# Kernel optimization log

Measured on AMD Instinct MI355X. Metric: run time of the kernel, lower is better.

The kernel has to match this reference:

```python
import jax, jax.numpy as jnp
import numpy as np

NMS_PRE, NMS_POST, NMS_THRESH = 1024, 512, 0.7
B, A, FEAT = 4, 70400, 27648
BN_EPS = 1e-5


def _bev_iou(boxes):
    # boxes: [K, 7] (x, y, z, dx, dy, dz, ry); axis-aligned BEV IoU
    x, y, dx, dy = boxes[:, 0], boxes[:, 1], boxes[:, 3], boxes[:, 4]
    x1, x2 = x - 0.5 * dx, x + 0.5 * dx
    y1, y2 = y - 0.5 * dy, y + 0.5 * dy
    iw = jnp.clip(jnp.minimum(x2[:, None], x2[None, :]) - jnp.maximum(x1[:, None], x1[None, :]), 0.0)
    ih = jnp.clip(jnp.minimum(y2[:, None], y2[None, :]) - jnp.maximum(y1[:, None], y1[None, :]), 0.0)
    inter = iw * ih
    area = dx * dy
    return inter / jnp.clip(area[:, None] + area[None, :] - inter, 1e-6)


def _greedy_nms(boxes, thresh):
    # boxes sorted by score desc; returns keep mask [K]
    K = boxes.shape[0]
    iou = _bev_iou(boxes)
    idx = jnp.arange(K)

    def step(keep, i):
        sup = (iou[i] > thresh) & (idx > i) & keep[i]
        return keep & ~sup, None

    keep, _ = jax.lax.scan(step, jnp.ones(K, dtype=bool), jnp.arange(K))
    return keep


def _proposal_one(box, cls):
    # box: [A, 7], cls: [A, n_cls]  ->  padded rois [NPOST,7], scores [NPOST], labels [NPOST]
    score = jnp.max(cls, axis=-1)
    label = jnp.argmax(cls, axis=-1)
    top_score, top_idx = jax.lax.top_k(score, NMS_PRE)
    top_box = box[top_idx]
    keep = _greedy_nms(top_box, NMS_THRESH)
    # stable: kept entries first, preserving score order
    order = jnp.argsort(jnp.where(keep, jnp.arange(NMS_PRE), NMS_PRE + jnp.arange(NMS_PRE)))
    sel = order[:NMS_POST]
    valid = jnp.arange(NMS_POST) < jnp.minimum(jnp.sum(keep), NMS_POST)
    rois = jnp.where(valid[:, None], top_box[sel], 0.0)
    roi_score = jnp.where(valid, top_score[sel], 0.0)
    roi_label = jnp.where(valid, label[top_idx][sel], 0) + 1  # +1 as in module
    return rois, roi_score, roi_label


def _bn_relu(h, g, b):
    # eval-mode BN with running_mean=0, running_var=1
    return jax.nn.relu(h * (g / jnp.sqrt(1.0 + BN_EPS)) + b)


def _decode(reg, anchors):
    # ResidualCoder_v1.decode_torch
    xa, ya, za = anchors[..., 0], anchors[..., 1], anchors[..., 2]
    dxa, dya, dza, ra = anchors[..., 3], anchors[..., 4], anchors[..., 5], anchors[..., 6]
    xt, yt, zt = reg[..., 0], reg[..., 1], reg[..., 2]
    dxt, dyt, dzt, rt = reg[..., 3], reg[..., 4], reg[..., 5], reg[..., 6]
    diag = jnp.sqrt(dxa * dxa + dya * dya)
    return jnp.stack([
        xt * diag + xa, yt * diag + ya, zt * dza + za,
        jnp.exp(dxt) * dxa, jnp.exp(dyt) * dya, jnp.exp(dzt) * dza,
        rt + ra], axis=-1)


def _rotate_z(box, ang):
    # rotate x,y of box [..., 7] by ang [...]
    c, s = jnp.cos(ang), jnp.sin(ang)
    x = box[..., 0] * c - box[..., 1] * s
    y = box[..., 0] * s + box[..., 1] * c
    return jnp.concatenate([x[..., None], y[..., None], box[..., 2:]], axis=-1)


def reference(rpn_box_preds, rpn_cls_preds, pooled_features,
              Ws1, g1, b1, Ws2, g2, b2,
              Wc1, gc1, bc1, Wc2, gc2, bc2, Wc3, bc3,
              Wr1, gr1, br1, Wr2, gr2, br2, Wr3, br3):
    # proposal_layer: per-batch topk + NMS + padded scatter (vmapped)
    rois, roi_scores, roi_labels = jax.vmap(_proposal_one)(rpn_box_preds, rpn_cls_preds)

    # shared / cls / reg heads (1x1 Conv1d == per-roi MLP), dropout off (eval)
    x = _bn_relu(pooled_features @ Ws1.T, g1, b1)
    x = _bn_relu(x @ Ws2.T, g2, b2)
    c = _bn_relu(x @ Wc1.T, gc1, bc1)
    c = _bn_relu(c @ Wc2.T, gc2, bc2)
    cls_preds = c @ Wc3.T + bc3          # [B*NPOST, 1]
    r = _bn_relu(x @ Wr1.T, gr1, br1)
    r = _bn_relu(r @ Wr2.T, gr2, br2)
    reg_preds = r @ Wr3.T + br3          # [B*NPOST, 7]

    bsz = rois.shape[0]
    cls_preds = cls_preds.reshape(bsz, -1, cls_preds.shape[-1])
    reg_preds = reg_preds.reshape(bsz, -1, 7)

    # generate_predict_box: decode against detached rois with xyz zeroed
    anchors = jax.lax.stop_gradient(rois)
    anchors = anchors.at[..., 0:3].set(0.0)
    box_ct = _decode(reg_preds, anchors)
    box_preds = _rotate_z(box_ct, rois[..., 6])
    box_preds = jnp.concatenate([box_preds[..., 0:3] + rois[..., 0:3], box_preds[..., 3:]], axis=-1)

    return jnp.concatenate([cls_preds, box_preds, roi_scores[..., None]], axis=-1)  # [B, NPOST, 9]


def setup_inputs():
    key = jax.random.key(0)
    ks = jax.random.split(key, 32)
    u = jax.random.uniform(ks[0], (B, A, 7), dtype=jnp.float32)
    lo = jnp.array([0.0, -40.0, -2.0, 1.5, 1.4, 1.0, -3.14159], jnp.float32)
    hi = jnp.array([70.0, 40.0, 0.0, 4.5, 2.0, 2.0, 3.14159], jnp.float32)
    rpn_box_preds = lo + u * (hi - lo)
    rpn_cls_preds = jax.random.normal(ks[1], (B, A, 3), dtype=jnp.float32)
    pooled_features = jax.random.normal(ks[2], (B * NMS_POST, FEAT), dtype=jnp.float32) * 0.1

    def w(k, o, i, std=None):
        s = (1.0 / np.sqrt(i)) if std is None else std
        return jax.random.normal(k, (o, i), dtype=jnp.float32) * s

    d = dict(
        rpn_box_preds=rpn_box_preds, rpn_cls_preds=rpn_cls_preds, pooled_features=pooled_features,
        Ws1=w(ks[3], 256, FEAT), g1=jnp.ones(256), b1=jnp.zeros(256),
        Ws2=w(ks[4], 256, 256), g2=jnp.ones(256), b2=jnp.zeros(256),
        Wc1=w(ks[5], 256, 256), gc1=jnp.ones(256), bc1=jnp.zeros(256),
        Wc2=w(ks[6], 256, 256), gc2=jnp.ones(256), bc2=jnp.zeros(256),
        Wc3=w(ks[7], 1, 256), bc3=jnp.zeros(1),
        Wr1=w(ks[8], 256, 256), gr1=jnp.ones(256), br1=jnp.zeros(256),
        Wr2=w(ks[9], 256, 256), gr2=jnp.ones(256), br2=jnp.zeros(256),
        Wr3=w(ks[10], 7, 256, std=0.001), br3=jnp.zeros(7),
    )
    return d
```

## Files before the change

kernel.cpp:

```cpp
#include <hip/hip_runtime.h>
#include <cstdint>

typedef unsigned int u32;
typedef unsigned long long u64;
typedef unsigned short u16;

#define BATCH 4
#define A_CNT 70400
#define FEAT 27648
#define KSPLIT 16
#define KCHUNK 1728
#define NTILE_IT 27

typedef __attribute__((ext_vector_type(8))) short bf16x8;
typedef __attribute__((ext_vector_type(4))) float f32x4;
typedef __attribute__((ext_vector_type(4))) u32 u32x4;

constexpr size_t OF_KEYS = 0;
constexpr size_t OF_TBOX = OF_KEYS + 1126400;
constexpr size_t OF_TSC  = OF_TBOX + 114688;
constexpr size_t OF_BX1  = OF_TSC + 16384;
constexpr size_t OF_BX2  = OF_BX1 + 16384;
constexpr size_t OF_BY1  = OF_BX2 + 16384;
constexpr size_t OF_BY2  = OF_BY1 + 16384;
constexpr size_t OF_BAR  = OF_BY2 + 16384;
constexpr size_t OF_MASK = OF_BAR + 16384;
constexpr size_t OF_ROIS = OF_MASK + 524288;
constexpr size_t OF_RSC  = OF_ROIS + 57344;
constexpr size_t OF_BSW  = OF_RSC + 8192;
constexpr size_t OF_PART = OF_BSW + 14155776;
constexpr size_t WS_NEED = OF_PART + 33554432;

__device__ __forceinline__ u32 keyOf(float f) {
  u32 u = __float_as_uint(f);
  return (u & 0x80000000u) ? ~u : (u | 0x80000000u);
}
__device__ __forceinline__ float keyToF(u32 k) {
  u32 u = (k & 0x80000000u) ? (k ^ 0x80000000u) : ~k;
  return __uint_as_float(u);
}
__device__ __forceinline__ u16 f2bf(float f) {
  u32 u = __float_as_uint(f);
  u32 r = 0x7FFFu + ((u >> 16) & 1u);
  return (u16)((u + r) >> 16);
}
__device__ __forceinline__ void gload_lds16(const void* g, void* l) {
  auto gp = reinterpret_cast<const __attribute__((address_space(1))) unsigned int*>(
      reinterpret_cast<uintptr_t>(g));
  auto lp = reinterpret_cast<__attribute__((address_space(3))) unsigned int*>(
      reinterpret_cast<uintptr_t>(l));
  __builtin_amdgcn_global_load_lds(gp, lp, 16, 0, 0);
}
__device__ __forceinline__ u64 shflx64(u64 v, int m) {
  u32 lo = (u32)v, hi = (u32)(v >> 32);
  lo = __shfl_xor(lo, m, 64);
  hi = __shfl_xor(hi, m, 64);
  return ((u64)hi << 32) | lo;
}
__device__ __forceinline__ u32x4 pack8(float4 a, float4 b) {
  u32x4 o;
  o.x = (u32)f2bf(a.x) | ((u32)f2bf(a.y) << 16);
  o.y = (u32)f2bf(a.z) | ((u32)f2bf(a.w) << 16);
  o.z = (u32)f2bf(b.x) | ((u32)f2bf(b.y) << 16);
  o.w = (u32)f2bf(b.z) | ((u32)f2bf(b.w) << 16);
  return o;
}
__device__ __forceinline__ bf16x8 cvt8(float4 a, float4 b) {
  u32x4 p = pack8(a, b);
  return *(bf16x8*)&p;
}

__global__ __launch_bounds__(1024) void k_fatA(const float* __restrict__ cls,
    const float* __restrict__ Ws1, u32* __restrict__ keys, u32* __restrict__ Bsw)
{
  int bid = blockIdx.x;
  int t = threadIdx.x;
  if (bid < 864) {
    u32 w = (u32)bid * 1024u + t;
    u32 tile = w >> 11;
    u32 rem = w & 2047u;
    u32 n = rem >> 3;
    u32 pq = (rem & 7u) << 4;
    u32 q0 = pq ^ ((n & 7u) << 4);
    u32 col0 = tile * 64u + (q0 >> 1);
    const float* src = Ws1 + (size_t)n * FEAT + col0;
    float4 f0 = *(const float4*)src;
    float4 f1 = *(const float4*)(src + 4);
    ((u32x4*)Bsw)[w] = pack8(f0, f1);
    return;
  }
  u32 g = (u32)(bid - 864) * 1024u + t;
  float s0 = cls[(size_t)g * 3 + 0];
  float s1 = cls[(size_t)g * 3 + 1];
  float s2 = cls[(size_t)g * 3 + 2];
  keys[g] = keyOf(fmaxf(s0, fmaxf(s1, s2)));
}

__global__ __launch_bounds__(1024) void k_prop(const u32* __restrict__ keys,
    const float* __restrict__ boxes, float* __restrict__ tbox, float* __restrict__ tsc,
    float* __restrict__ bx1, float* __restrict__ bx2, float* __restrict__ by1,
    float* __restrict__ by2, float* __restrict__ bar)
{
  int b = blockIdx.x, t = threadIdx.x;
  int lane = t & 63, wv = t >> 6;
  const u32* kb = keys + (size_t)b * A_CNT;
  __shared__ u64 s[2048];
  __shared__ u32 partials[16];
  __shared__ u32 cc;
  u32 h[35];
#pragma unroll
  for (int j = 0; j < 35; ++j) {
    int g0 = t + ((2 * j) << 10);
    int g1 = t + ((2 * j + 1) << 10);
    u32 a = (g0 < A_CNT) ? (kb[g0] >> 16) : 0u;
    u32 c2 = (g1 < A_CNT) ? (kb[g1] >> 16) : 0u;
    h[j] = a | (c2 << 16);
  }
  if (t == 0) cc = 0u;
  u32 lo = 0, hi = 65536;
  while (hi - lo > 1) {
    u32 mid = (lo + hi) >> 1;
    u32 c = 0;
#pragma unroll
    for (int j = 0; j < 35; ++j) {
      c += ((h[j] & 0xFFFFu) >= mid) ? 1u : 0u;
      c += ((h[j] >> 16) >= mid) ? 1u : 0u;
    }
#pragma unroll
    for (int o = 32; o > 0; o >>= 1) c += __shfl_xor(c, o, 64);
    __syncthreads();
    if (lane == 0) partials[wv] = c;
    __syncthreads();
    u32 tot = 0;
#pragma unroll
    for (int w2 = 0; w2 < 16; ++w2) tot += partials[w2];
    if (tot >= 1024u) lo = mid; else hi = mid;
  }
  u32 kth = lo;
  __syncthreads();
  u32 kc = kb[t];
#pragma unroll 1
  for (int i = 0; i < 69; ++i) {
    int g = t + (i << 10);
    u32 k = kc;
    if (i < 68) {
      int gn = t + ((i + 1) << 10);
      kc = (gn < A_CNT) ? kb[gn] : 0u;
    }
    bool pass = (g < A_CNT) && ((k >> 16) >= kth);
    u64 mm = __ballot(pass);
    if (mm) {
      int leader = __ffsll((unsigned long long)mm) - 1;
      u32 base = 0;
      if (lane == leader) base = atomicAdd(&cc, (u32)__popcll(mm));
      base = __shfl(base, leader, 64);
      if (pass) {
        u32 pos = base + (u32)__popcll(mm & ((1ull << lane) - 1ull));
        if (pos < 2048u) s[pos] = ((u64)k << 32) | (u32)(~(u32)g);
      }
    }
  }
  __syncthreads();
  u32 m = cc; if (m > 2048u) m = 2048u;
  for (int e = t; e < 2048; e += 1024) if (e >= (int)m) s[e] = 0ull;
  __syncthreads();
  {
    u64 v0 = s[2 * t], v1 = s[2 * t + 1];
#pragma unroll
    for (u32 k = 2; k <= 128; k <<= 1) {
      bool desc = ((t & (k >> 1)) == 0);
#pragma unroll
      for (u32 j = (k >> 1); j >= 2; j >>= 1) {
        u32 mmk = j >> 1;
        u64 p0 = shflx64(v0, mmk);
        u64 p1 = shflx64(v1, mmk);
        bool up = ((t & mmk) == 0);
        bool mx = (desc == up);
        v0 = mx ? (v0 > p0 ? v0 : p0) : (v0 < p0 ? v0 : p0);
        v1 = mx ? (v1 > p1 ? v1 : p1) : (v1 < p1 ? v1 : p1);
      }
      if (desc ? (v0 < v1) : (v0 > v1)) { u64 tmp = v0; v0 = v1; v1 = tmp; }
    }
    s[2 * t] = v0; s[2 * t + 1] = v1;
    __syncthreads();
    for (u32 k = 256; k <= 2048; k <<= 1) {
      for (u32 j = k >> 1; j >= 128; j >>= 1) {
        for (int e = t; e < 2048; e += 1024) {
          u32 p = (u32)e ^ j;
          if (p > (u32)e) {
            bool d2 = ((e & k) == 0);
            u64 x = s[e], y = s[p];
            if (d2 ? (x < y) : (x > y)) { s[e] = y; s[p] = x; }
          }
        }
        __syncthreads();
      }
      u64 v0 = s[2 * t], v1 = s[2 * t + 1];
      bool desc = ((t & (k >> 1)) == 0);
#pragma unroll
      for (u32 j = 64; j >= 2; j >>= 1) {
        u32 mmk = j >> 1;
        u64 p0 = shflx64(v0, mmk);
        u64 p1 = shflx64(v1, mmk);
        bool up = ((t & mmk) == 0);
        bool mx = (desc == up);
        v0 = mx ? (v0 > p0 ? v0 : p0) : (v0 < p0 ? v0 : p0);
        v1 = mx ? (v1 > p1 ? v1 : p1) : (v1 < p1 ? v1 : p1);
      }
      if (desc ? (v0 < v1) : (v0 > v1)) { u64 tmp = v0; v0 = v1; v1 = tmp; }
      s[2 * t] = v0; s[2 * t + 1] = v1;
      __syncthreads();
    }
  }
  u64 comp = s[t];
  u32 kk = (u32)(comp >> 32);
  u32 a = ~(u32)(comp & 0xFFFFFFFFull);
  int o = b * 1024 + t;
  tsc[o] = keyToF(kk);
  const float* bp = boxes + ((size_t)b * A_CNT + a) * 7;
  float x = bp[0], y = bp[1], z = bp[2], dx = bp[3], dy = bp[4], dz = bp[5], rr = bp[6];
  float* tb = tbox + (size_t)o * 7;
  tb[0] = x; tb[1] = y; tb[2] = z; tb[3] = dx; tb[4] = dy; tb[5] = dz; tb[6] = rr;
  {
#pragma clang fp contract(off)
    bx1[o] = x - 0.5f * dx; bx2[o] = x + 0.5f * dx;
    by1[o] = y - 0.5f * dy; by2[o] = y + 0.5f * dy;
    bar[o] = dx * dy;
  }
}

__global__ __launch_bounds__(256) void k_fatB(const float* __restrict__ A,
    const u32* __restrict__ Bsw, float* __restrict__ part,
    const float* __restrict__ bx1, const float* __restrict__ bx2,
    const float* __restrict__ by1, const float* __restrict__ by2,
    const float* __restrict__ bar, u32* __restrict__ mask)
{
  __shared__ __align__(16) char smem[65536];
  int bid = blockIdx.x;
  if (bid >= 512) {
    int mi = bid - 512;
    int b = mi >> 6;
    int cbk = (mi >> 2) & 15;
    int rb0 = (mi & 3) * 4;
    int tt = threadIdx.x;
    int rbi = tt >> 6, ln = tt & 63;
    int r = (rb0 + rbi) * 64 + ln;
    int o = b * 1024, jc0 = cbk * 64;
    float* cx1 = (float*)(smem);
    float* cx2 = (float*)(smem + 256);
    float* cy1 = (float*)(smem + 512);
    float* cy2 = (float*)(smem + 768);
    float* car = (float*)(smem + 1024);
    if (tt < 64) {
      cx1[tt] = bx1[o + jc0 + tt]; cx2[tt] = bx2[o + jc0 + tt];
      cy1[tt] = by1[o + jc0 + tt]; cy2[tt] = by2[o + jc0 + tt];
      car[tt] = bar[o + jc0 + tt];
    }
    __syncthreads();
    float rx1 = bx1[o + r], rx2 = bx2[o + r], ry1 = by1[o + r], ry2 = by2[o + r], rar = bar[o + r];
    u32 w0 = 0, w1 = 0;
    {
#pragma clang fp contract(off)
      for (int c = 0; c < 64; ++c) {
        int jc = jc0 + c;
        float iw = fminf(rx2, cx2[c]) - fmaxf(rx1, cx1[c]); iw = fmaxf(iw, 0.0f);
        float ih = fminf(ry2, cy2[c]) - fmaxf(ry1, cy1[c]); ih = fmaxf(ih, 0.0f);
        float inter = iw * ih;
        float den = fmaxf(rar + car[c] - inter, 1e-6f);
        float iou = inter / den;
        if ((iou > 0.7f) && (jc > r)) {
          if (c < 32) w0 |= 1u << c; else w1 |= 1u << (c - 32);
        }
      }
    }
    mask[((size_t)(o + r)) * 32 + cbk * 2 + 0] = w0;
    mask[((size_t)(o + r)) * 32 + cbk * 2 + 1] = w1;
    return;
  }
  int q = bid >> 3;
  int ks = (bid & 7) * 2 + (q >> 5);
  int mt = q & 31;
  int tid = threadIdx.x, lane = tid & 63, wv = tid >> 6;
  int row16 = lane & 15, kgrp = lane >> 4;

  f32x4 acc[16];
#pragma unroll
  for (int i = 0; i < 16; ++i) acc[i] = (f32x4){0.f, 0.f, 0.f, 0.f};

  const float* aptr = A + ((size_t)(mt * 64 + wv * 16 + row16)) * FEAT
                        + (size_t)ks * KCHUNK + kgrp * 8;
  const char* bsrc_base = (const char*)Bsw + ((size_t)(ks * NTILE_IT)) * 32768 + (wv * 8) * 1024 + lane * 16;
  int bdoff = (wv * 8) * 1024;

  int boff[16][2];
#pragma unroll
  for (int ksub = 0; ksub < 2; ++ksub) {
    int qq = ksub * 64 + kgrp * 16;
#pragma unroll
    for (int nf = 0; nf < 16; ++nf) {
      int n = nf * 16 + row16;
      boff[nf][ksub] = n * 128 + (qq ^ ((n & 7) << 4));
    }
  }

  bf16x8 a0, a1;
  {
    const float4* ap = (const float4*)aptr;
    float4 g0 = ap[0], g1 = ap[1];
    const float4* ap2 = (const float4*)(aptr + 32);
    float4 g2 = ap2[0], g3 = ap2[1];
    a0 = cvt8(g0, g1);
    a1 = cvt8(g2, g3);
#pragma unroll
    for (int i = 0; i < 8; ++i)
      gload_lds16(bsrc_base + i * 1024, smem + bdoff + i * 1024);
  }
  __syncthreads();

  for (int it = 0; it < NTILE_IT; ++it) {
    char* Bcur = smem + ((it & 1) ? 32768 : 0);
    char* Bnxt = smem + ((it & 1) ? 0 : 32768);
    bool has = (it + 1 < NTILE_IT);
    float4 g0, g1, g2, g3;
    if (has) {
      const float* an = aptr + (it + 1) * 64;
      const float4* ap = (const float4*)an;
      g0 = ap[0]; g1 = ap[1];
      const float4* ap2 = (const float4*)(an + 32);
      g2 = ap2[0]; g3 = ap2[1];
      const char* bs = bsrc_base + (size_t)(it + 1) * 32768;
#pragma unroll
      for (int i = 0; i < 8; ++i)
        gload_lds16(bs + i * 1024, Bnxt + bdoff + i * 1024);
    }
#pragma unroll
    for (int nf = 0; nf < 16; ++nf) {
      bf16x8 b0 = *(const bf16x8*)(Bcur + boff[nf][0]);
      acc[nf] = __builtin_amdgcn_mfma_f32_16x16x32_bf16(a0, b0, acc[nf], 0, 0, 0);
      bf16x8 b1 = *(const bf16x8*)(Bcur + boff[nf][1]);
      acc[nf] = __builtin_amdgcn_mfma_f32_16x16x32_bf16(a1, b1, acc[nf], 0, 0, 0);
    }
    if (has) {
      a0 = cvt8(g0, g1);
      a1 = cvt8(g2, g3);
    }
    __syncthreads();
  }
  float* pb = part + (size_t)ks * 524288;
  int orow = mt * 64 + wv * 16 + kgrp * 4;
#pragma unroll
  for (int nf = 0; nf < 16; ++nf) {
    int col = nf * 16 + row16;
#pragma unroll
    for (int rr = 0; rr < 4; ++rr)
      pb[(size_t)(orow + rr) * 256 + col] = acc[nf][rr];
  }
}

__global__ __launch_bounds__(64) void k_nms(const u32* __restrict__ mask,
    const float* __restrict__ tbox, const float* __restrict__ tsc,
    float* __restrict__ rois, float* __restrict__ rsc)
{
  int b = blockIdx.x;
  int lane = threadIdx.x;
  int el = lane & 31;
  const u32* M = mask + (size_t)b * 1024 * 32;
  u32 R = 0;
  u32 cur[32], nxt[32];
#pragma unroll
  for (int i = 0; i < 32; ++i) cur[i] = M[(size_t)(i * 32 + el)];
#pragma unroll 1
  for (int c = 0; c < 32; ++c) {
    if (c < 31) {
      int nb = (c + 1) * 1024 + el;
#pragma unroll
      for (int i = 0; i < 32; ++i) nxt[i] = M[(size_t)(nb + i * 32)];
    }
    u32 w = R;
#pragma unroll
    for (int i = 0; i < 32; ++i) w |= ((w >> i) & 1u) ? 0u : cur[i];
    u32 wfin = __shfl(w, c, 64);
#pragma unroll
    for (int i = 0; i < 32; ++i) R |= ((wfin >> i) & 1u) ? 0u : cur[i];
#pragma unroll
    for (int i = 0; i < 32; ++i) cur[i] = nxt[i];
  }
  u32 keepw = (lane < 32) ? ~R : 0u;
  int c = __popc(keepw);
  int pre = c;
  for (int d = 1; d < 64; d <<= 1) {
    int v = __shfl_up(pre, d, 64);
    if (lane >= d) pre += v;
  }
  int total = __shfl(pre, 31, 64);
  int base = pre - c;
  if (lane < 32) {
    u32 w = keepw;
    int rank = base;
    while (w) {
      int bit = __ffs(w) - 1;
      w &= w - 1;
      if (rank < 512) {
        int r = lane * 32 + bit;
        const float* tb = tbox + ((size_t)b * 1024 + r) * 7;
        float* rp = rois + ((size_t)b * 512 + rank) * 7;
        rp[0] = tb[0]; rp[1] = tb[1]; rp[2] = tb[2]; rp[3] = tb[3];
        rp[4] = tb[4]; rp[5] = tb[5]; rp[6] = tb[6];
        rsc[b * 512 + rank] = tsc[b * 1024 + r];
      }
      rank++;
    }
  }
  for (int z = total + lane; z < 512; z += 64) {
    float* rp = rois + ((size_t)b * 512 + z) * 7;
    rp[0] = rp[1] = rp[2] = rp[3] = rp[4] = rp[5] = rp[6] = 0.0f;
    rsc[b * 512 + z] = 0.0f;
  }
}

__device__ __forceinline__ void layer4(const float (*IN)[256], const float* __restrict__ W,
    const float* __restrict__ g, const float* __restrict__ bb, float (*OUT)[256], int t, int h)
{
  float acc[4] = {0, 0, 0, 0};
  const float* Wrow = W + (size_t)t * 256;
  for (int k = 0; k < 256; k += 4) {
    float4 w4 = *(const float4*)&Wrow[k];
#pragma unroll
    for (int r = 0; r < 4; ++r) {
      float4 xv = *(const float4*)&IN[h * 4 + r][k];
      acc[r] = fmaf(xv.x, w4.x, acc[r]);
      acc[r] = fmaf(xv.y, w4.y, acc[r]);
      acc[r] = fmaf(xv.z, w4.z, acc[r]);
      acc[r] = fmaf(xv.w, w4.w, acc[r]);
    }
  }
  float sc = g[t] / sqrtf(1.0f + 1e-5f);
  float bv = bb[t];
#pragma unroll
  for (int r = 0; r < 4; ++r)
    OUT[h * 4 + r][t] = fmaxf(fmaf(acc[r], sc, bv), 0.0f);
}

__global__ __launch_bounds__(512) void k_chain(const float* __restrict__ part,
    const float* __restrict__ Ws2, const float* __restrict__ Wc1, const float* __restrict__ Wc2,
    const float* __restrict__ Wr1, const float* __restrict__ Wr2,
    const float* __restrict__ g1, const float* __restrict__ b1,
    const float* __restrict__ g2, const float* __restrict__ b2,
    const float* __restrict__ gc1, const float* __restrict__ bc1,
    const float* __restrict__ gc2, const float* __restrict__ bc2,
    const float* __restrict__ gr1, const float* __restrict__ br1,
    const float* __restrict__ gr2, const float* __restrict__ br2,
    const float* __restrict__ Wc3, const float* __restrict__ bc3,
    const float* __restrict__ Wr3, const float* __restrict__ br3,
    const float* __restrict__ rois, const float* __restrict__ rsc,
    float* __restrict__ out)
{
  int bid = blockIdx.x, tid = threadIdx.x;
  int t = tid & 255, h = tid >> 8;
  __shared__ __align__(16) float bufX[8][256];
  __shared__ __align__(16) float bufY[8][256];
  __shared__ __align__(16) float bufC[8][256];
  __shared__ __align__(16) float bufR[8][256];
  __shared__ float hd[64];
  {
    float sc = g1[t] / sqrtf(1.0f + 1e-5f);
    float bv = b1[t];
#pragma unroll
    for (int r = 0; r < 4; ++r) {
      int row = h * 4 + r;
      float s = 0.f;
#pragma unroll
      for (int ks = 0; ks < KSPLIT; ++ks)
        s += part[(size_t)ks * 524288 + (size_t)(bid * 8 + row) * 256 + t];
      bufX[row][t] = fmaxf(fmaf(s, sc, bv), 0.0f);
    }
  }
  __syncthreads();
  layer4(bufX, Ws2, g2, b2, bufY, t, h);
  __syncthreads();
  layer4(bufY, Wc1, gc1, bc1, bufC, t, h);
  layer4(bufY, Wr1, gr1, br1, bufR, t, h);
  __syncthreads();
  layer4(bufC, Wc2, gc2, bc2, bufX, t, h);
  layer4(bufR, Wr2, gr2, br2, bufY, t, h);
  __syncthreads();
  int wv = tid >> 6, ln = tid & 63;
  for (int task = wv; task < 64; task += 8) {
    float p;
    if (task < 8) {
      float4 yv = *(const float4*)&bufX[task][ln * 4];
      float4 w4 = ((const float4*)Wc3)[ln];
      p = yv.x * w4.x + yv.y * w4.y + yv.z * w4.z + yv.w * w4.w;
    } else {
      int i = task - 8, row = i / 7, j = i % 7;
      float4 yv = *(const float4*)&bufY[row][ln * 4];
      float4 w4 = ((const float4*)(Wr3 + j * 256))[ln];
      p = yv.x * w4.x + yv.y * w4.y + yv.z * w4.z + yv.w * w4.w;
    }
#pragma unroll
    for (int off = 32; off > 0; off >>= 1) p += __shfl_xor(p, off, 64);
    if (ln == 0) hd[task] = p;
  }
  __syncthreads();
  if (tid < 8) {
    int m = bid * 8 + tid;
    float clsv = hd[tid] + bc3[0];
    float rg[7];
#pragma unroll
    for (int j = 0; j < 7; ++j) rg[j] = hd[8 + tid * 7 + j] + br3[j];
    const float* R = rois + (size_t)m * 7;
    float rx = R[0], ry = R[1], rz = R[2], dxa = R[3], dya = R[4], dza = R[5], ra = R[6];
    float diag = sqrtf(dxa * dxa + dya * dya);
    float x = rg[0] * diag, y = rg[1] * diag, z = rg[2] * dza;
    float ex = expf(rg[3]) * dxa, ey = expf(rg[4]) * dya, ez = expf(rg[5]) * dza;
    float hr = rg[6] + ra;
    float cc = cosf(ra), sn = sinf(ra);
    float xr = x * cc - y * sn, yr = x * sn + y * cc;
    float* O = out + (size_t)m * 9;
    O[0] = clsv; O[1] = xr + rx; O[2] = yr + ry; O[3] = z + rz;
    O[4] = ex; O[5] = ey; O[6] = ez; O[7] = hr; O[8] = rsc[m];
  }
}

extern "C" void kernel_launch(void* const* d_in, const int* in_sizes, int n_in,
                              void* d_out, int out_size, void* d_ws, size_t ws_size,
                              hipStream_t stream)
{
  const float* rpn_box = (const float*)d_in[0];
  const float* rpn_cls = (const float*)d_in[1];
  const float* pooled  = (const float*)d_in[2];
  const float* Ws1 = (const float*)d_in[3];
  const float* g1  = (const float*)d_in[4];
  const float* b1  = (const float*)d_in[5];
  const float* Ws2 = (const float*)d_in[6];
  const float* g2  = (const float*)d_in[7];
  const float* b2  = (const float*)d_in[8];
  const float* Wc1 = (const float*)d_in[9];
  const float* gc1 = (const float*)d_in[10];
  const float* bc1 = (const float*)d_in[11];
  const float* Wc2 = (const float*)d_in[12];
  const float* gc2 = (const float*)d_in[13];
  const float* bc2 = (const float*)d_in[14];
  const float* Wc3 = (const float*)d_in[15];
  const float* bc3 = (const float*)d_in[16];
  const float* Wr1 = (const float*)d_in[17];
  const float* gr1 = (const float*)d_in[18];
  const float* br1 = (const float*)d_in[19];
  const float* Wr2 = (const float*)d_in[20];
  const float* gr2 = (const float*)d_in[21];
  const float* br2 = (const float*)d_in[22];
  const float* Wr3 = (const float*)d_in[23];
  const float* br3 = (const float*)d_in[24];

  if (ws_size < WS_NEED) return;

  char* ws = (char*)d_ws;
  u32* keys = (u32*)(ws + OF_KEYS);
  float* tbox = (float*)(ws + OF_TBOX);
  float* tsc  = (float*)(ws + OF_TSC);
  float* bx1 = (float*)(ws + OF_BX1);
  float* bx2 = (float*)(ws + OF_BX2);
  float* by1 = (float*)(ws + OF_BY1);
  float* by2 = (float*)(ws + OF_BY2);
  float* bar = (float*)(ws + OF_BAR);
  u32* mask = (u32*)(ws + OF_MASK);
  float* roisb = (float*)(ws + OF_ROIS);
  float* rscb  = (float*)(ws + OF_RSC);
  u32* Bsw = (u32*)(ws + OF_BSW);
  float* part = (float*)(ws + OF_PART);

  k_fatA<<<1139, 1024, 0, stream>>>(rpn_cls, Ws1, keys, Bsw);
  k_prop<<<4, 1024, 0, stream>>>(keys, rpn_box, tbox, tsc, bx1, bx2, by1, by2, bar);
  k_fatB<<<768, 256, 0, stream>>>(pooled, Bsw, part, bx1, bx2, by1, by2, bar, mask);
  k_nms<<<4, 64, 0, stream>>>(mask, tbox, tsc, roisb, rscb);
  k_chain<<<256, 512, 0, stream>>>(part, Ws2, Wc1, Wc2, Wr1, Wr2,
                                   g1, b1, g2, b2, gc1, bc1, gc2, bc2,
                                   gr1, br1, gr2, br2, Wc3, bc3, Wr3, br3,
                                   roisb, rscb, (float*)d_out);
}
```

Baseline: 266.1 us.

## Fuse top-k proposal selection with the big GEMM and split IoU mask kernel

The 4-block proposal/top-k kernel is merged into the large split-K GEMM launch, so the serial sort runs alongside GEMM blocks instead of in its own near-empty launch. The GEMM tile is restructured into 1024-thread blocks: 16 waves each own a 16-column slice, and the A tile is staged in LDS as bf16 while B is double-buffered in LDS. The IoU mask computation moves out of the GEMM kernel into its own 1024-thread kernel that runs after proposal selection. The restructured GEMM adds extra barriers per iteration and uses 72KB of LDS per block, which may lower occupancy, and the mask work now costs an additional launch.

```diff
diff --git a/kernel.cpp b/kernel.cpp
--- a/kernel.cpp
+++ b/kernel.cpp
@@ -14,6 +14,7 @@
 
 typedef __attribute__((ext_vector_type(8))) short bf16x8;
 typedef __attribute__((ext_vector_type(4))) float f32x4;
+typedef __attribute__((ext_vector_type(2))) u32 u32x2;
 typedef __attribute__((ext_vector_type(4))) u32 u32x4;
 
 constexpr size_t OF_KEYS = 0;
@@ -64,10 +65,6 @@
   o.z = (u32)f2bf(b.x) | ((u32)f2bf(b.y) << 16);
   o.w = (u32)f2bf(b.z) | ((u32)f2bf(b.w) << 16);
   return o;
-}
-__device__ __forceinline__ bf16x8 cvt8(float4 a, float4 b) {
-  u32x4 p = pack8(a, b);
-  return *(bf16x8*)&p;
 }
 
 __global__ __launch_bounds__(1024) void k_fatA(const float* __restrict__ cls,
@@ -96,265 +93,267 @@
   keys[g] = keyOf(fmaxf(s0, fmaxf(s1, s2)));
 }
 
-__global__ __launch_bounds__(1024) void k_prop(const u32* __restrict__ keys,
-    const float* __restrict__ boxes, float* __restrict__ tbox, float* __restrict__ tsc,
+__global__ __launch_bounds__(1024) void k_big(const u32* __restrict__ keys,
+    const float* __restrict__ boxes, const float* __restrict__ A,
+    const u32* __restrict__ Bsw, float* __restrict__ part,
+    float* __restrict__ tbox, float* __restrict__ tsc,
     float* __restrict__ bx1, float* __restrict__ bx2, float* __restrict__ by1,
     float* __restrict__ by2, float* __restrict__ bar)
 {
-  int b = blockIdx.x, t = threadIdx.x;
-  int lane = t & 63, wv = t >> 6;
-  const u32* kb = keys + (size_t)b * A_CNT;
-  __shared__ u64 s[2048];
-  __shared__ u32 partials[16];
-  __shared__ u32 cc;
-  u32 h[35];
-#pragma unroll
-  for (int j = 0; j < 35; ++j) {
-    int g0 = t + ((2 * j) << 10);
-    int g1 = t + ((2 * j + 1) << 10);
-    u32 a = (g0 < A_CNT) ? (kb[g0] >> 16) : 0u;
-    u32 c2 = (g1 < A_CNT) ? (kb[g1] >> 16) : 0u;
-    h[j] = a | (c2 << 16);
-  }
-  if (t == 0) cc = 0u;
-  u32 lo = 0, hi = 65536;
-  while (hi - lo > 1) {
-    u32 mid = (lo + hi) >> 1;
-    u32 c = 0;
+  __shared__ __align__(16) char smem[73728];
+  int bid = blockIdx.x;
+  int t = threadIdx.x;
+  if (bid < 4) {
+    int b = bid;
+    int lane = t & 63, wv = t >> 6;
+    const u32* kb = keys + (size_t)b * A_CNT;
+    u64* s = (u64*)smem;
+    u32* partials = (u32*)(smem + 16384);
+    u32* ccp = (u32*)(smem + 16448);
+    u32 h[35];
 #pragma unroll
     for (int j = 0; j < 35; ++j) {
-      c += ((h[j] & 0xFFFFu) >= mid) ? 1u : 0u;
-      c += ((h[j] >> 16) >= mid) ? 1u : 0u;
-    }
-#pragma unroll
-    for (int o = 32; o > 0; o >>= 1) c += __shfl_xor(c, o, 64);
+      int g0 = t + ((2 * j) << 10);
+      int g1 = t + ((2 * j + 1) << 10);
+      u32 a = (g0 < A_CNT) ? (kb[g0] >> 16) : 0u;
+      u32 c2 = (g1 < A_CNT) ? (kb[g1] >> 16) : 0u;
+      h[j] = a | (c2 << 16);
+    }
+    if (t == 0) ccp[0] = 0u;
+    u32 lo = 0, hi = 65536;
+    while (hi - lo > 1) {
+      u32 mid = (lo + hi) >> 1;
+      u32 c = 0;
+#pragma unroll
+      for (int j = 0; j < 35; ++j) {
+        c += ((h[j] & 0xFFFFu) >= mid) ? 1u : 0u;
+        c += ((h[j] >> 16) >= mid) ? 1u : 0u;
+      }
+#pragma unroll
+      for (int o = 32; o > 0; o >>= 1) c += __shfl_xor(c, o, 64);
+      __syncthreads();
+      if (lane == 0) partials[wv] = c;
+      __syncthreads();
+      u32 tot = 0;
+#pragma unroll
+      for (int w2 = 0; w2 < 16; ++w2) tot += partials[w2];
+      if (tot >= 1024u) lo = mid; else hi = mid;
+    }
+    u32 kth = lo;
     __syncthreads();
-    if (lane == 0) partials[wv] = c;
+    u32 kc = kb[t];
+#pragma unroll 1
+    for (int i = 0; i < 69; ++i) {
+      int g = t + (i << 10);
+      u32 k = kc;
+      if (i < 68) {
+        int gn = t + ((i + 1) << 10);
+        kc = (gn < A_CNT) ? kb[gn] : 0u;
+      }
+      bool pass = (g < A_CNT) && ((k >> 16) >= kth);
+      u64 mm = __ballot(pass);
+      if (mm) {
+        int leader = __ffsll((unsigned long long)mm) - 1;
+        u32 base = 0;
+        if (lane == leader) base = atomicAdd(ccp, (u32)__popcll(mm));
+        base = __shfl(base, leader, 64);
+        if (pass) {
+          u32 pos = base + (u32)__popcll(mm & ((1ull << lane) - 1ull));
+          if (pos < 2048u) s[pos] = ((u64)k << 32) | (u32)(~(u32)g);
+        }
+      }
+    }
     __syncthreads();
-    u32 tot = 0;
-#pragma unroll
-    for (int w2 = 0; w2 < 16; ++w2) tot += partials[w2];
-    if (tot >= 1024u) lo = mid; else hi = mid;
-  }
-  u32 kth = lo;
-  __syncthreads();
-  u32 kc = kb[t];
-#pragma unroll 1
-  for (int i = 0; i < 69; ++i) {
-    int g = t + (i << 10);
-    u32 k = kc;
-    if (i < 68) {
-      int gn = t + ((i + 1) << 10);
-      kc = (gn < A_CNT) ? kb[gn] : 0u;
-    }
-    bool pass = (g < A_CNT) && ((k >> 16) >= kth);
-    u64 mm = __ballot(pass);
-    if (mm) {
-      int leader = __ffsll((unsigned long long)mm) - 1;
-      u32 base = 0;
-      if (lane == leader) base = atomicAdd(&cc, (u32)__popcll(mm));
-      base = __shfl(base, leader, 64);
-      if (pass) {
-        u32 pos = base + (u32)__popcll(mm & ((1ull << lane) - 1ull));
-        if (pos < 2048u) s[pos] = ((u64)k << 32) | (u32)(~(u32)g);
-      }
-    }
-  }
-  __syncthreads();
-  u32 m = cc; if (m > 2048u) m = 2048u;
-  for (int e = t; e < 2048; e += 1024) if (e >= (int)m) s[e] = 0ull;
-  __syncthreads();
-  {
-    u64 v0 = s[2 * t], v1 = s[2 * t + 1];
-#pragma unroll
-    for (u32 k = 2; k <= 128; k <<= 1) {
-      bool desc = ((t & (k >> 1)) == 0);
-#pragma unroll
-      for (u32 j = (k >> 1); j >= 2; j >>= 1) {
-        u32 mmk = j >> 1;
-        u64 p0 = shflx64(v0, mmk);
-        u64 p1 = shflx64(v1, mmk);
-        bool up = ((t & mmk) == 0);
-        bool mx = (desc == up);
-        v0 = mx ? (v0 > p0 ? v0 : p0) : (v0 < p0 ? v0 : p0);
-        v1 = mx ? (v1 > p1 ? v1 : p1) : (v1 < p1 ? v1 : p1);
-      }
-      if (desc ? (v0 < v1) : (v0 > v1)) { u64 tmp = v0; v0 = v1; v1 = tmp; }
-    }
-    s[2 * t] = v0; s[2 * t + 1] = v1;
+    u32 m = ccp[0]; if (m > 2048u) m = 2048u;
+    for (int e = t; e < 2048; e += 1024) if (e >= (int)m) s[e] = 0ull;
     __syncthreads();
-    for (u32 k = 256; k <= 2048; k <<= 1) {
-      for (u32 j = k >> 1; j >= 128; j >>= 1) {
-        for (int e = t; e < 2048; e += 1024) {
-          u32 p = (u32)e ^ j;
-          if (p > (u32)e) {
-            bool d2 = ((e & k) == 0);
-            u64 x = s[e], y = s[p];
-            if (d2 ? (x < y) : (x > y)) { s[e] = y; s[p] = x; }
-          }
+    {
+      u64 v0 = s[2 * t], v1 = s[2 * t + 1];
+#pragma unroll
+      for (u32 k = 2; k <= 128; k <<= 1) {
+        bool desc = ((t & (k >> 1)) == 0);
+#pragma unroll
+        for (u32 j = (k >> 1); j >= 2; j >>= 1) {
+          u32 mmk = j >> 1;
+          u64 p0 = shflx64(v0, mmk);
+          u64 p1 = shflx64(v1, mmk);
+          bool up = ((t & mmk) == 0);
+          bool mx = (desc == up);
+          v0 = mx ? (v0 > p0 ? v0 : p0) : (v0 < p0 ? v0 : p0);
+          v1 = mx ? (v1 > p1 ? v1 : p1) : (v1 < p1 ? v1 : p1);
         }
-        __syncthreads();
-      }
-      u64 v0 = s[2 * t], v1 = s[2 * t + 1];
-      bool desc = ((t & (k >> 1)) == 0);
-#pragma unroll
-      for (u32 j = 64; j >= 2; j >>= 1) {
-        u32 mmk = j >> 1;
-        u64 p0 = shflx64(v0, mmk);
-        u64 p1 = shflx64(v1, mmk);
-        bool up = ((t & mmk) == 0);
-        bool mx = (desc == up);
-        v0 = mx ? (v0 > p0 ? v0 : p0) : (v0 < p0 ? v0 : p0);
-        v1 = mx ? (v1 > p1 ? v1 : p1) : (v1 < p1 ? v1 : p1);
-      }
-      if (desc ? (v0 < v1) : (v0 > v1)) { u64 tmp = v0; v0 = v1; v1 = tmp; }
+        if (desc ? (v0 < v1) : (v0 > v1)) { u64 tmp = v0; v0 = v1; v1 = tmp; }
+      }
       s[2 * t] = v0; s[2 * t + 1] = v1;
       __syncthreads();
-    }
-  }
-  u64 comp = s[t];
-  u32 kk = (u32)(comp >> 32);
-  u32 a = ~(u32)(comp & 0xFFFFFFFFull);
-  int o = b * 1024 + t;
-  tsc[o] = keyToF(kk);
-  const float* bp = boxes + ((size_t)b * A_CNT + a) * 7;
-  float x = bp[0], y = bp[1], z = bp[2], dx = bp[3], dy = bp[4], dz = bp[5], rr = bp[6];
-  float* tb = tbox + (size_t)o * 7;
-  tb[0] = x; tb[1] = y; tb[2] = z; tb[3] = dx; tb[4] = dy; tb[5] = dz; tb[6] = rr;
+      for (u32 k = 256; k <= 2048; k <<= 1) {
+        for (u32 j = k >> 1; j >= 128; j >>= 1) {
+          for (int e = t; e < 2048; e += 1024) {
+            u32 p = (u32)e ^ j;
+            if (p > (u32)e) {
+              bool d2 = ((e & k) == 0);
+              u64 x = s[e], y = s[p];
+              if (d2 ? (x < y) : (x > y)) { s[e] = y; s[p] = x; }
+            }
+          }
+          __syncthreads();
+        }
+        u64 v0 = s[2 * t], v1 = s[2 * t + 1];
+        bool desc = ((t & (k >> 1)) == 0);
+#pragma unroll
+        for (u32 j = 64; j >= 2; j >>= 1) {
+          u32 mmk = j >> 1;
+          u64 p0 = shflx64(v0, mmk);
+          u64 p1 = shflx64(v1, mmk);
+          bool up = ((t & mmk) == 0);
+          bool mx = (desc == up);
+          v0 = mx ? (v0 > p0 ? v0 : p0) : (v0 < p0 ? v0 : p0);
+          v1 = mx ? (v1 > p1 ? v1 : p1) : (v1 < p1 ? v1 : p1);
+        }
+        if (desc ? (v0 < v1) : (v0 > v1)) { u64 tmp = v0; v0 = v1; v1 = tmp; }
+        s[2 * t] = v0; s[2 * t + 1] = v1;
+        __syncthreads();
+      }
+    }
+    u64 comp = s[t];
+    u32 kk = (u32)(comp >> 32);
+    u32 a = ~(u32)(comp & 0xFFFFFFFFull);
+    int o = b * 1024 + t;
+    tsc[o] = keyToF(kk);
+    const float* bp = boxes + ((size_t)b * A_CNT + a) * 7;
+    float x = bp[0], y = bp[1], z = bp[2], dx = bp[3], dy = bp[4], dz = bp[5], rr = bp[6];
+    float* tb = tbox + (size_t)o * 7;
+    tb[0] = x; tb[1] = y; tb[2] = z; tb[3] = dx; tb[4] = dy; tb[5] = dz; tb[6] = rr;
+    {
+#pragma clang fp contract(off)
+      bx1[o] = x - 0.5f * dx; bx2[o] = x + 0.5f * dx;
+      by1[o] = y - 0.5f * dy; by2[o] = y + 0.5f * dy;
+      bar[o] = dx * dy;
+    }
+    return;
+  }
+  int bid2 = bid - 4;
+  int q = bid2 >> 3;
+  int ks = (bid2 & 7) * 2 + (q >> 5);
+  int mt = q & 31;
+  int lane = t & 63, wvid = t >> 6;
+  int row16 = lane & 15, kgrp = lane >> 4;
+
+  f32x4 acc[4];
+#pragma unroll
+  for (int i = 0; i < 4; ++i) acc[i] = (f32x4){0.f, 0.f, 0.f, 0.f};
+
+  int arow = t >> 4;
+  int akb = (t & 15) * 4;
+  const float* ap_base = A + ((size_t)(mt * 64 + arow)) * FEAT + (size_t)ks * KCHUNK + akb;
+  int asw = (arow & 7) << 4;
+  int awoff = arow * 128 + (((t & 15) * 8) ^ asw);
+  const char* bsrc_base = (const char*)Bsw + ((size_t)(ks * NTILE_IT)) * 32768 + wvid * 2048 + lane * 16;
+  int bdoff = wvid * 2048 + lane * 16;
+  char* Albuf = smem;
+  char* Bbase = smem + 8192;
+
+  int aoff[4][2], boff[2];
+#pragma unroll
+  for (int ksub = 0; ksub < 2; ++ksub) {
+    int qq = ksub * 64 + kgrp * 16;
+#pragma unroll
+    for (int mf = 0; mf < 4; ++mf) {
+      int row = mf * 16 + row16;
+      aoff[mf][ksub] = row * 128 + (qq ^ ((row & 7) << 4));
+    }
+    int n = wvid * 16 + row16;
+    boff[ksub] = n * 128 + (qq ^ ((n & 7) << 4));
+  }
+
+  {
+    float4 ga = *(const float4*)ap_base;
+    u32x2 c;
+    c.x = (u32)f2bf(ga.x) | ((u32)f2bf(ga.y) << 16);
+    c.y = (u32)f2bf(ga.z) | ((u32)f2bf(ga.w) << 16);
+    *(u32x2*)(Albuf + awoff) = c;
+    gload_lds16(bsrc_base, Bbase + bdoff);
+    gload_lds16(bsrc_base + 1024, Bbase + bdoff + 1024);
+  }
+  __syncthreads();
+
+  for (int it = 0; it < NTILE_IT; ++it) {
+    char* Bcur = Bbase + ((it & 1) ? 32768 : 0);
+    char* Bnxt = Bbase + ((it & 1) ? 0 : 32768);
+    bool has = (it + 1 < NTILE_IT);
+    float4 ga;
+    if (has) ga = *(const float4*)(ap_base + (it + 1) * 64);
+    bf16x8 bf0 = *(const bf16x8*)(Bcur + boff[0]);
+    bf16x8 bf1 = *(const bf16x8*)(Bcur + boff[1]);
+    __syncthreads();
+    if (has) {
+      const char* bs = bsrc_base + (size_t)(it + 1) * 32768;
+      gload_lds16(bs, Bnxt + bdoff);
+      gload_lds16(bs + 1024, Bnxt + bdoff + 1024);
+    }
+#pragma unroll
+    for (int mf = 0; mf < 4; ++mf) {
+      bf16x8 a0 = *(const bf16x8*)(Albuf + aoff[mf][0]);
+      acc[mf] = __builtin_amdgcn_mfma_f32_16x16x32_bf16(a0, bf0, acc[mf], 0, 0, 0);
+      bf16x8 a1 = *(const bf16x8*)(Albuf + aoff[mf][1]);
+      acc[mf] = __builtin_amdgcn_mfma_f32_16x16x32_bf16(a1, bf1, acc[mf], 0, 0, 0);
+    }
+    __syncthreads();
+    if (has) {
+      u32x2 c;
+      c.x = (u32)f2bf(ga.x) | ((u32)f2bf(ga.y) << 16);
+      c.y = (u32)f2bf(ga.z) | ((u32)f2bf(ga.w) << 16);
+      *(u32x2*)(Albuf + awoff) = c;
+    }
+    __syncthreads();
+  }
+  float* pb = part + (size_t)ks * 524288;
+#pragma unroll
+  for (int mf = 0; mf < 4; ++mf) {
+    int orow = mt * 64 + mf * 16 + kgrp * 4;
+    int col = wvid * 16 + row16;
+#pragma unroll
+    for (int rr = 0; rr < 4; ++rr)
+      pb[(size_t)(orow + rr) * 256 + col] = acc[mf][rr];
+  }
+}
+
+__global__ __launch_bounds__(1024) void k_mask(const float* __restrict__ bx1,
+    const float* __restrict__ bx2, const float* __restrict__ by1,
+    const float* __restrict__ by2, const float* __restrict__ bar,
+    u32* __restrict__ mask)
+{
+  __shared__ float csm[16][5][64];
+  int tt = threadIdx.x;
+  int ug = tt >> 6, ln = tt & 63;
+  int unit = blockIdx.x * 16 + ug;
+  int b = unit >> 8, cbk = (unit >> 4) & 15, rb = unit & 15;
+  int o = b * 1024, jc0 = cbk * 64;
+  int r = rb * 64 + ln;
+  csm[ug][0][ln] = bx1[o + jc0 + ln];
+  csm[ug][1][ln] = bx2[o + jc0 + ln];
+  csm[ug][2][ln] = by1[o + jc0 + ln];
+  csm[ug][3][ln] = by2[o + jc0 + ln];
+  csm[ug][4][ln] = bar[o + jc0 + ln];
+  __syncthreads();
+  float rx1 = bx1[o + r], rx2 = bx2[o + r], ry1 = by1[o + r], ry2 = by2[o + r], rar = bar[o + r];
+  u32 w0 = 0, w1 = 0;
   {
 #pragma clang fp contract(off)
-    bx1[o] = x - 0.5f * dx; bx2[o] = x + 0.5f * dx;
-    by1[o] = y - 0.5f * dy; by2[o] = y + 0.5f * dy;
-    bar[o] = dx * dy;
-  }
-}
-
-__global__ __launch_bounds__(256) void k_fatB(const float* __restrict__ A,
-    const u32* __restrict__ Bsw, float* __restrict__ part,
-    const float* __restrict__ bx1, const float* __restrict__ bx2,
-    const float* __restrict__ by1, const float* __restrict__ by2,
-    const float* __restrict__ bar, u32* __restrict__ mask)
-{
-  __shared__ __align__(16) char smem[65536];
-  int bid = blockIdx.x;
-  if (bid >= 512) {
-    int mi = bid - 512;
-    int b = mi >> 6;
-    int cbk = (mi >> 2) & 15;
-    int rb0 = (mi & 3) * 4;
-    int tt = threadIdx.x;
-    int rbi = tt >> 6, ln = tt & 63;
-    int r = (rb0 + rbi) * 64 + ln;
-    int o = b * 1024, jc0 = cbk * 64;
-    float* cx1 = (float*)(smem);
-    float* cx2 = (float*)(smem + 256);
-    float* cy1 = (float*)(smem + 512);
-    float* cy2 = (float*)(smem + 768);
-    float* car = (float*)(smem + 1024);
-    if (tt < 64) {
-      cx1[tt] = bx1[o + jc0 + tt]; cx2[tt] = bx2[o + jc0 + tt];
-      cy1[tt] = by1[o + jc0 + tt]; cy2[tt] = by2[o + jc0 + tt];
-      car[tt] = bar[o + jc0 + tt];
-    }
-    __syncthreads();
-    float rx1 = bx1[o + r], rx2 = bx2[o + r], ry1 = by1[o + r], ry2 = by2[o + r], rar = bar[o + r];
-    u32 w0 = 0, w1 = 0;
-    {
-#pragma clang fp contract(off)
-      for (int c = 0; c < 64; ++c) {
-        int jc = jc0 + c;
-        float iw = fminf(rx2, cx2[c]) - fmaxf(rx1, cx1[c]); iw = fmaxf(iw, 0.0f);
-        float ih = fminf(ry2, cy2[c]) - fmaxf(ry1, cy1[c]); ih = fmaxf(ih, 0.0f);
-        float inter = iw * ih;
-        float den = fmaxf(rar + car[c] - inter, 1e-6f);
-        float iou = inter / den;
-        if ((iou > 0.7f) && (jc > r)) {
-          if (c < 32) w0 |= 1u << c; else w1 |= 1u << (c - 32);
-        }
-      }
-    }
-    mask[((size_t)(o + r)) * 32 + cbk * 2 + 0] = w0;
-    mask[((size_t)(o + r)) * 32 + cbk * 2 + 1] = w1;
-    return;
-  }
-  int q = bid >> 3;
-  int ks = (bid & 7) * 2 + (q >> 5);
-  int mt = q & 31;
-  int tid = threadIdx.x, lane = tid & 63, wv = tid >> 6;
-  int row16 = lane & 15, kgrp = lane >> 4;
-
-  f32x4 acc[16];
-#pragma unroll
-  for (int i = 0; i < 16; ++i) acc[i] = (f32x4){0.f, 0.f, 0.f, 0.f};
-
-  const float* aptr = A + ((size_t)(mt * 64 + wv * 16 + row16)) * FEAT
-                        + (size_t)ks * KCHUNK + kgrp * 8;
-  const char* bsrc_base = (const char*)Bsw + ((size_t)(ks * NTILE_IT)) * 32768 + (wv * 8) * 1024 + lane * 16;
-  int bdoff = (wv * 8) * 1024;
-
-  int boff[16][2];
-#pragma unroll
-  for (int ksub = 0; ksub < 2; ++ksub) {
-    int qq = ksub * 64 + kgrp * 16;
-#pragma unroll
-    for (int nf = 0; nf < 16; ++nf) {
-      int n = nf * 16 + row16;
-      boff[nf][ksub] = n * 128 + (qq ^ ((n & 7) << 4));
-    }
-  }
-
-  bf16x8 a0, a1;
-  {
-    const float4* ap = (const float4*)aptr;
-    float4 g0 = ap[0], g1 = ap[1];
-    const float4* ap2 = (const float4*)(aptr + 32);
-    float4 g2 = ap2[0], g3 = ap2[1];
-    a0 = cvt8(g0, g1);
-    a1 = cvt8(g2, g3);
-#pragma unroll
-    for (int i = 0; i < 8; ++i)
-      gload_lds16(bsrc_base + i * 1024, smem + bdoff + i * 1024);
-  }
-  __syncthreads();
-
-  for (int it = 0; it < NTILE_IT; ++it) {
-    char* Bcur = smem + ((it & 1) ? 32768 : 0);
-    char* Bnxt = smem + ((it & 1) ? 0 : 32768);
-    bool has = (it + 1 < NTILE_IT);
-    float4 g0, g1, g2, g3;
-    if (has) {
-      const float* an = aptr + (it + 1) * 64;
-      const float4* ap = (const float4*)an;
-      g0 = ap[0]; g1 = ap[1];
-      const float4* ap2 = (const float4*)(an + 32);
-      g2 = ap2[0]; g3 = ap2[1];
-      const char* bs = bsrc_base + (size_t)(it + 1) * 32768;
-#pragma unroll
-      for (int i = 0; i < 8; ++i)
-        gload_lds16(bs + i * 1024, Bnxt + bdoff + i * 1024);
-    }
-#pragma unroll
-    for (int nf = 0; nf < 16; ++nf) {
-      bf16x8 b0 = *(const bf16x8*)(Bcur + boff[nf][0]);
-      acc[nf] = __builtin_amdgcn_mfma_f32_16x16x32_bf16(a0, b0, acc[nf], 0, 0, 0);
-      bf16x8 b1 = *(const bf16x8*)(Bcur + boff[nf][1]);
-      acc[nf] = __builtin_amdgcn_mfma_f32_16x16x32_bf16(a1, b1, acc[nf], 0, 0, 0);
-    }
-    if (has) {
-      a0 = cvt8(g0, g1);
-      a1 = cvt8(g2, g3);
-    }
-    __syncthreads();
-  }
-  float* pb = part + (size_t)ks * 524288;
-  int orow = mt * 64 + wv * 16 + kgrp * 4;
-#pragma unroll
-  for (int nf = 0; nf < 16; ++nf) {
-    int col = nf * 16 + row16;
-#pragma unroll
-    for (int rr = 0; rr < 4; ++rr)
-      pb[(size_t)(orow + rr) * 256 + col] = acc[nf][rr];
-  }
+    for (int c = 0; c < 64; ++c) {
+      int jc = jc0 + c;
+      float iw = fminf(rx2, csm[ug][1][c]) - fmaxf(rx1, csm[ug][0][c]); iw = fmaxf(iw, 0.0f);
+      float ih = fminf(ry2, csm[ug][3][c]) - fmaxf(ry1, csm[ug][2][c]); ih = fmaxf(ih, 0.0f);
+      float inter = iw * ih;
+      float den = fmaxf(rar + csm[ug][4][c] - inter, 1e-6f);
+      float iou = inter / den;
+      if ((iou > 0.7f) && (jc > r)) {
+        if (c < 32) w0 |= 1u << c; else w1 |= 1u << (c - 32);
+      }
+    }
+  }
+  mask[((size_t)(o + r)) * 32 + cbk * 2 + 0] = w0;
+  mask[((size_t)(o + r)) * 32 + cbk * 2 + 1] = w1;
 }
 
 __global__ __launch_bounds__(64) void k_nms(const u32* __restrict__ mask,
@@ -570,8 +569,9 @@
   float* part = (float*)(ws + OF_PART);
 
   k_fatA<<<1139, 1024, 0, stream>>>(rpn_cls, Ws1, keys, Bsw);
-  k_prop<<<4, 1024, 0, stream>>>(keys, rpn_box, tbox, tsc, bx1, bx2, by1, by2, bar);
-  k_fatB<<<768, 256, 0, stream>>>(pooled, Bsw, part, bx1, bx2, by1, by2, bar, mask);
+  k_big<<<516, 1024, 0, stream>>>(keys, rpn_box, pooled, Bsw, part,
+                                  tbox, tsc, bx1, bx2, by1, by2, bar);
+  k_mask<<<64, 1024, 0, stream>>>(bx1, bx2, by1, by2, bar, mask);
   k_nms<<<4, 64, 0, stream>>>(mask, tbox, tsc, roisb, rscb);
   k_chain<<<256, 512, 0, stream>>>(part, Ws2, Wc1, Wc2, Wr1, Wr2,
                                    g1, b1, g2, b2, gc1, bc1, gc2, bc2,
```

Measured after the change: 258.5 us. 2.8% less time.
